# Kernel optimization log

Hardware: AMD Instinct MI355X
Metric: run time of the kernel (lower is better)

## Reference

```python
import jax, jax.numpy as jnp
import numpy as np

B, CITY, H, E, IN = 512, 100, 256, 256, 2
D2 = 2 * H  # num_directions * hidden_size
PEN = 1e6   # already_played_penalty


def _cell(x, h, c, Wih, Whh, b):
    # PyTorch LSTM cell, gate order i,f,g,o
    g = x @ Wih.T + h @ Whh.T + b
    i, f, gg, o = jnp.split(g, 4, axis=-1)
    c = jax.nn.sigmoid(f) * c + jax.nn.sigmoid(i) * jnp.tanh(gg)
    h = jax.nn.sigmoid(o) * jnp.tanh(c)
    return h, c


def _run_lstm(xs, Wih, Whh, b, reverse):
    # xs: [B, T, E] -> outputs [B, T, H], final (h, c)
    Bsz, hdim = xs.shape[0], Whh.shape[1]
    init = (jnp.zeros((Bsz, hdim), xs.dtype), jnp.zeros((Bsz, hdim), xs.dtype))
    def step(carry, x):
        h, c = _cell(x, carry[0], carry[1], Wih, Whh, b)
        return (h, c), h
    (h, c), hs = jax.lax.scan(step, init, jnp.swapaxes(xs, 0, 1), reverse=reverse)
    return jnp.swapaxes(hs, 0, 1), h, c


def setup_inputs() -> dict:
    key = jax.random.key(0)
    ks = iter(jax.random.split(key, 32))
    nrm = lambda shape: 0.1 * jax.random.normal(next(ks), shape, dtype=jnp.float32)
    return {
        "inputs": jax.random.normal(next(ks), (B, CITY, IN), dtype=jnp.float32),
        "test_roads": jax.random.randint(next(ks), (B, CITY), 0, CITY, dtype=jnp.int32),
        "W_embed": nrm((E, IN)),
        "enc_Wih_f": nrm((4 * H, E)), "enc_Whh_f": nrm((4 * H, H)), "enc_b_f": nrm((4 * H,)),
        "enc_Wih_b": nrm((4 * H, E)), "enc_Whh_b": nrm((4 * H, H)), "enc_b_b": nrm((4 * H,)),
        "dec_Wih_f": nrm((4 * H, D2)), "dec_Whh_f": nrm((4 * H, H)), "dec_b_f": nrm((4 * H,)),
        "dec_Wih_b": nrm((4 * H, D2)), "dec_Whh_b": nrm((4 * H, H)), "dec_b_b": nrm((4 * H,)),
        "W_ref": nrm((D2, D2)), "W_q": nrm((D2, D2)), "v": nrm((D2,)),
        "W_ref2": nrm((D2, D2)), "W_q2": nrm((D2, D2)), "v2": nrm((D2,)),
    }


def _forward(inputs, test_roads, W_embed,
             enc_Wih_f, enc_Whh_f, enc_b_f, enc_Wih_b, enc_Whh_b, enc_b_b,
             dec_Wih_f, dec_Whh_f, dec_b_f, dec_Wih_b, dec_Whh_b, dec_b_b,
             W_ref, W_q, v, W_ref2, W_q2, v2):
    Bsz, city, _ = inputs.shape
    emb = inputs @ W_embed.T                                  # [B, city, E]
    enc_f, hf0, cf0 = _run_lstm(emb, enc_Wih_f, enc_Whh_f, enc_b_f, False)
    enc_b, hb0, cb0 = _run_lstm(emb, enc_Wih_b, enc_Whh_b, enc_b_b, True)
    Enc = jnp.concatenate([enc_f, enc_b], axis=-1)            # [B, city, D2]
    # dropout p=0 -> Enc is loop-invariant; hoist the two ref projections
    ref1 = Enc @ W_ref.T                                      # [B, city, D2]
    ref2 = Enc @ W_ref2.T                                     # [B, city, D2]

    def step(carry, tgt):
        x, hf, cf, hb, cb, played, loss = carry
        hf, cf = _cell(x, hf, cf, dec_Wih_f, dec_Whh_f, dec_b_f)
        hb, cb = _cell(x, hb, cb, dec_Wih_b, dec_Whh_b, dec_b_b)
        dec_out = jnp.concatenate([hf, hb], axis=-1)          # [B, D2]
        ow = jnp.tanh(ref1 + (dec_out @ W_q.T)[:, None, :]) @ v - PEN * played   # [B, city]
        aw = jax.nn.softmax(jnp.tanh(ref2 + (x @ W_q2.T)[:, None, :]) @ v2, axis=1)
        sel = jnp.argmax(ow, axis=1)                          # [B]
        x_new = jnp.einsum('bj,bjk->bk', aw, Enc)             # [B, D2]
        played = played + jax.nn.one_hot(sel, city, dtype=played.dtype)
        ce = jax.nn.logsumexp(ow, axis=1) - jnp.take_along_axis(ow, tgt[:, None], axis=1)[:, 0]
        return (x_new, hf, cf, hb, cb, played, loss + ce), None

    x0 = jnp.zeros((Bsz, Enc.shape[-1]), inputs.dtype)
    played0 = jnp.zeros((Bsz, city), inputs.dtype)
    loss0 = jnp.zeros((Bsz,), inputs.dtype)
    carry, _ = jax.lax.scan(step, (x0, hf0, cf0, hb0, cb0, played0, loss0),
                            test_roads.T.astype(jnp.int32))
    return carry[-1]                                          # path_loss [B]


def reference(inputs, test_roads, W_embed,
              enc_Wih_f, enc_Whh_f, enc_b_f, enc_Wih_b, enc_Whh_b, enc_b_b,
              dec_Wih_f, dec_Whh_f, dec_b_f, dec_Wih_b, dec_Whh_b, dec_b_b,
              W_ref, W_q, v, W_ref2, W_q2, v2):
    return _forward(inputs, test_roads, W_embed,
                    enc_Wih_f, enc_Whh_f, enc_b_f, enc_Wih_b, enc_Whh_b, enc_b_b,
                    dec_Wih_f, dec_Whh_f, dec_b_f, dec_Wih_b, dec_Whh_b, dec_b_b,
                    W_ref, W_q, v, W_ref2, W_q2, v2)
```

## Files before the change

### kernel.cpp

```cpp
#include <hip/hip_runtime.h>
#include <hip/hip_fp16.h>
#include <math.h>

namespace {
constexpr int Bn  = 512;
constexpr int Tn  = 100;
constexpr int Hn  = 256;
constexpr int En  = 256;
constexpr int D2n = 512;
constexpr int G4n = 1024;
constexpr float PENf = 1e6f;
constexpr size_t BIGN = (size_t)Bn * Tn * D2n;
constexpr int FLAG_STRIDE = 32;
constexpr int EBLK = 512;
constexpr int DBLK = 896;
constexpr size_t BAR_UINTS = (EBLK + DBLK) * FLAG_STRIDE + 64;
}

using short8  = __attribute__((ext_vector_type(8))) short;
using us8     = __attribute__((ext_vector_type(8))) unsigned short;
using floatx4 = __attribute__((ext_vector_type(4))) float;

template<typename T> __device__ __forceinline__ float cvt_to_f(T x);
template<> __device__ __forceinline__ float cvt_to_f<float>(float x) { return x; }
template<> __device__ __forceinline__ float cvt_to_f<__half>(__half x) {
  return __half2float(x);
}
template<typename T> __device__ __forceinline__ T cvt_from_f(float x);
template<> __device__ __forceinline__ float cvt_from_f<float>(float x) { return x; }
template<> __device__ __forceinline__ __half cvt_from_f<__half>(float x) {
  return __float2half(x);
}
__device__ __forceinline__ float h2f_bits(unsigned short b) {
  __half_raw r; r.x = b; return __half2float(__half(r));
}
__device__ __forceinline__ float fast_exp(float x) {
  return __builtin_amdgcn_exp2f(x * 1.44269504088896340736f);
}
__device__ __forceinline__ float sigmoidf(float x) {
  return __builtin_amdgcn_rcpf(1.0f + fast_exp(-x));
}
__device__ __forceinline__ float fast_tanhf(float x) {
  return 1.0f - 2.0f * __builtin_amdgcn_rcpf(fast_exp(2.0f * x) + 1.0f);
}

__device__ __forceinline__ float loadf_dev(const float* p) {
  return __uint_as_float(__hip_atomic_load((const unsigned*)p, __ATOMIC_RELAXED,
                                           __HIP_MEMORY_SCOPE_AGENT));
}
// ... 49 lines not shown
  split2(v.z, h2, l2); split2(v.w, h3, l3);
  *(short4*)hp = make_short4(h0, h1, h2, h3);
  *(short4*)lp = make_short4(l0, l1, l2, l3);
}

template<int NB>
__device__ __forceinline__ void grid_syncN(unsigned* flags, unsigned* release,
                                           unsigned no) {
  __builtin_amdgcn_s_waitcnt(0);
  __syncthreads();
  if (blockIdx.x == 0) {
    for (int i = threadIdx.x; i < NB; i += 256) {
      if (i > 0) {
        while (__hip_atomic_load(&flags[i * FLAG_STRIDE], __ATOMIC_RELAXED,
                                 __HIP_MEMORY_SCOPE_AGENT) < no)
          __builtin_amdgcn_s_sleep(1);
      }
    }
    __syncthreads();
    if (threadIdx.x == 0)
      __hip_atomic_store(release, no, __ATOMIC_RELAXED, __HIP_MEMORY_SCOPE_AGENT);
  } else {
    if (threadIdx.x == 0) {
      __hip_atomic_store(&flags[blockIdx.x * FLAG_STRIDE], no, __ATOMIC_RELAXED,
                         __HIP_MEMORY_SCOPE_AGENT);
      while (__hip_atomic_load(release, __ATOMIC_RELAXED,
                               __HIP_MEMORY_SCOPE_AGENT) < no)
        __builtin_amdgcn_s_sleep(2);
    }
    __syncthreads();
  }
}

template<typename CT, bool ACC, int NT, bool CSC>
__device__ __forceinline__ void gemm64v2(short* smem,
    const float* A, int lda, int m0,
    const float* B, int ldb, int n0, int K,
    CT* Cbase, size_t crstride, int tid) {
  constexpr int BPL  = NT * 128;
  constexpr int BSZ  = NT * 512;
  constexpr int BUFS = 4096 + 2 * BSZ;
  const int lane = tid & 63, wave = tid >> 6, qm = lane & 15, quad = lane >> 4;
  const int ra = tid >> 3, c4 = tid & 7, j0 = (c4 & 1) * 4, gq = c4 >> 1;
  const int a0 = gq * 512 + ra * 8 + j0;
  const int a1 = gq * 512 + (ra + 32) * 8 + j0;
  const int b0 = gq * BPL + ra * 8 + j0;
  const int b1 = gq * BPL + (ra + 32) * 8 + j0;
  const int CN = K >> 5;

  floatx4 acc[NT];
#pragma unroll
  for (int nt = 0; nt < NT; ++nt) acc[nt] = (floatx4){0.f, 0.f, 0.f, 0.f};

  float4 Aa0, Aa1, Ba0, Ba1, Ab0, Ab1, Bb0, Bb1;
  auto ld = [&](int c, float4& x0, float4& x1, float4& y0, float4& y1) {
    const int k0 = c * 32 + c4 * 4;
    x0 = load4_dev(A + (size_t)(m0 + ra) * lda + k0);
    x1 = load4_dev(A + (size_t)(m0 + ra + 32) * lda + k0);
    y0 = *(const float4*)(B + (size_t)(n0 + ra) * ldb + k0);
    if (NT == 4)
      y1 = *(const float4*)(B + (size_t)(n0 + ra + 32) * ldb + k0);
  };
  auto st = [&](short* bp, const float4& x0, const float4& x1,
                const float4& y0, const float4& y1) {
    store4split(x0, bp + a0, bp + 2048 + a0);
    store4split(x1, bp + a1, bp + 2048 + a1);
    store4split(y0, bp + 4096 + b0, bp + 4096 + BSZ + b0);
    if (NT == 4) store4split(y1, bp + 4096 + b1, bp + 4096 + BSZ + b1);
  };
  auto mm = [&](const short* bp) {
    const int abase = quad * 512 + (wave * 16 + qm) * 8;
    const short8 ah = *(const short8*)&bp[abase];
    const short8 al = *(const short8*)&bp[2048 + abase];
#pragma unroll
    for (int nt = 0; nt < NT; ++nt) {
      const int bb = quad * BPL + (nt * 16 + qm) * 8;
      const short8 bh = *(const short8*)&bp[4096 + bb];
      const short8 bl = *(const short8*)&bp[4096 + BSZ + bb];
      acc[nt] = __builtin_amdgcn_mfma_f32_16x16x32_bf16(ah, bh, acc[nt], 0, 0, 0);
      acc[nt] = __builtin_amdgcn_mfma_f32_16x16x32_bf16(ah, bl, acc[nt], 0, 0, 0);
      acc[nt] = __builtin_amdgcn_mfma_f32_16x16x32_bf16(al, bh, acc[nt], 0, 0, 0);
    }
  };

  ld(0, Aa0, Aa1, Ba0, Ba1);
  if (CN > 1) ld(1, Ab0, Ab1, Bb0, Bb1);
  st(smem, Aa0, Aa1, Ba0, Ba1);
  __syncthreads();
  for (int c = 0; c < CN; c += 2) {
    if (c + 2 < CN) ld(c + 2, Aa0, Aa1, Ba0, Ba1);
    mm(smem);
    if (c + 1 < CN) st(smem + BUFS, Ab0, Ab1, Bb0, Bb1);
    __syncthreads();
    if (c + 1 < CN) {
      if (c + 3 < CN) ld(c + 3, Ab0, Ab1, Bb0, Bb1);
      mm(smem + BUFS);
      if (c + 2 < CN) st(smem, Aa0, Aa1, Ba0, Ba1);
      __syncthreads();
    }
  }

#pragma unroll
  for (int nt = 0; nt < NT; ++nt)
#pragma unroll
    for (int r2 = 0; r2 < 4; ++r2) {
      const int m = wave * 16 + quad * 4 + r2, n = nt * 16 + qm;
      CT* cp = Cbase + (size_t)m * crstride + n;
      float o = acc[nt][r2];
      if (CSC) {
        if (ACC) o += cvt_to_f<CT>(load_dev<CT>(cp));
        store_dev<CT>(cp, cvt_from_f<CT>(o));
      } else {
        if (ACC) o += cvt_to_f<CT>(*cp);
        *cp = cvt_from_f<CT>(o);
      }
    }
}

__device__ __forceinline__ void gates_gemm_v2(floatx4 acc[4], short* smem,
    const float* A1, int lda1, const float* B1, int ldb1, int K1,
    const float* A2, int lda2, const float* B2, int ldb2, int K2,
    int m0, int hoff, int tid) {
  const int lane = tid & 63, wave = tid >> 6, qm = lane & 15, quad = lane >> 4;
  const int ra = tid >> 3, c4 = tid & 7, j0 = (c4 & 1) * 4, gq = c4 >> 1;
  const int a0 = gq * 512 + ra * 8 + j0;
  const int a1 = gq * 512 + (ra + 32) * 8 + j0;
  const int g0 = (ra >> 4) * Hn + hoff + (ra & 15);
  const int g1 = ((ra + 32) >> 4) * Hn + hoff + ((ra + 32) & 15);
  const int C1 = K1 >> 5;
  const int C2 = A2 ? (K2 >> 5) : 0;
  const int CN = C1 + C2;

  float4 Aa0, Aa1, Ba0, Ba1, Ab0, Ab1, Bb0, Bb1;
  auto ld = [&](int c, float4& x0, float4& x1, float4& y0, float4& y1) {
    const float* A; const float* B; int lda, ldb, k0;
    if (c < C1) { A = A1; B = B1; lda = lda1; ldb = ldb1; k0 = c * 32; }
    else        { A = A2; B = B2; lda = lda2; ldb = ldb2; k0 = (c - C1) * 32; }
    k0 += c4 * 4;
    x0 = load4_dev(A + (size_t)(m0 + ra) * lda + k0);
    x1 = load4_dev(A + (size_t)(m0 + ra + 32) * lda + k0);
    y0 = *(const float4*)(B + (size_t)g0 * ldb + k0);
    y1 = *(const float4*)(B + (size_t)g1 * ldb + k0);
  };
  auto st2 = [&](short* bp, const float4& x0, const float4& x1,
                 const float4& y0, const float4& y1) {
    store4split(x0, bp + a0, bp + 2048 + a0);
    store4split(x1, bp + a1, bp + 2048 + a1);
    store4split(y0, bp + 4096 + a0, bp + 6144 + a0);
    store4split(y1, bp + 4096 + a1, bp + 6144 + a1);
  };
  auto mm = [&](const short* bp) {
    const int abase = quad * 512 + (wave * 16 + qm) * 8;
    const short8 ah = *(const short8*)&bp[abase];
    const short8 al = *(const short8*)&bp[2048 + abase];
#pragma unroll
    for (int gg = 0; gg < 4; ++gg) {
      const int bb = quad * 512 + (gg * 16 + qm) * 8;
      const short8 bh = *(const short8*)&bp[4096 + bb];
      const short8 bl = *(const short8*)&bp[6144 + bb];
      acc[gg] = __builtin_amdgcn_mfma_f32_16x16x32_bf16(ah, bh, acc[gg], 0, 0, 0);
      acc[gg] = __builtin_amdgcn_mfma_f32_16x16x32_bf16(ah, bl, acc[gg], 0, 0, 0);
      acc[gg] = __builtin_amdgcn_mfma_f32_16x16x32_bf16(al, bh, acc[gg], 0, 0, 0);
    }
  };

  if (CN <= 0) return;
  ld(0, Aa0, Aa1, Ba0, Ba1);
  if (CN > 1) ld(1, Ab0, Ab1, Bb0, Bb1);
  st2(smem, Aa0, Aa1, Ba0, Ba1);
  __syncthreads();
  for (int c = 0; c < CN; c += 2) {
    if (c + 2 < CN) ld(c + 2, Aa0, Aa1, Ba0, Ba1);
    mm(smem);
    if (c + 1 < CN) st2(smem + 8192, Ab0, Ab1, Bb0, Bb1);
    __syncthreads();
    if (c + 1 < CN) {
      if (c + 3 < CN) ld(c + 3, Ab0, Ab1, Bb0, Bb1);
      mm(smem + 8192);
      if (c + 2 < CN) st2(smem, Aa0, Aa1, Ba0, Ba1);
      __syncthreads();
    }
  }
}

__global__ void weff_kernel(const float* Wih_f, const float* Wih_b,
                            const float* W_embed, float* weff_f, float* weff_b) {
  const int gidx = blockIdx.x * 256 + threadIdx.x;
  if (gidx >= G4n) return;
  float f0 = 0.f, f1 = 0.f, b0 = 0.f, b1 = 0.f;
  for (int e = 0; e < En; ++e) {
    const float w0 = W_embed[e * 2 + 0];
    const float w1 = W_embed[e * 2 + 1];
    const float wf = Wih_f[gidx * En + e];
    const float wb = Wih_b[gidx * En + e];
    f0 = fmaf(wf, w0, f0); f1 = fmaf(wf, w1, f1);
    b0 = fmaf(wb, w0, b0); b1 = fmaf(wb, w1, b1);
  }
  weff_f[gidx * 2 + 0] = f0; weff_f[gidx * 2 + 1] = f1;
  weff_b[gidx * 2 + 0] = b0; weff_b[gidx * 2 + 1] = b1;
}

template<typename ET, typename RT1, typename RT2>
struct EncP {
  const float* inputs;
  const float* Whh_f; const float* Whh_b;
  const float* b_f; const float* b_b;
  const float* weff_f; const float* weff_b;
  const float* W_ref; const float* W_ref2;
  float* hbuf;
  float* c_dec;
  float* dec_out0;
  ET* Enc; RT1* ref1; RT2* ref2;
  unsigned* flags; unsigned* release;
};

template<typename ET, typename RT1, typename RT2>
__global__ __launch_bounds__(256, 2) void enc_coop(EncP<ET, RT1, RT2> P) {
  __shared__ __align__(16) short smem[16384];
  const int bid = blockIdx.x, tid = threadIdx.x;
  const bool gr = bid < 256;
  const int dir = (bid >> 7) & 1, btile = (bid >> 4) & 7, hs = bid & 15;
// ... 63 lines not shown
        const float hn = sigmoidf(gv[3][r2]) * fast_tanhf(cn);
        h_reg[r2] = hn;
        const int m = btile * 64 + wave * 16 + quad * 4 + r2;
        storef_dev(&hdst[(size_t)m * Hn + hcol], hn);
        store_dev<ET>(&P.Enc[(size_t)m * Tn * D2n + (size_t)tt * D2n + dir * Hn + hcol],
                      cvt_from_f<ET>(hn));
      }
    } else if (t > 0) {
      ref_job(hprev, r_dir ? (Tn - t) : (t - 1));
    }
    grid_syncN<EBLK>(P.flags, P.release, ++sync_no);
  }
  if (!gr) {
    ref_job(P.hbuf + (size_t)1 * (2 * Bn * Hn), r_dir ? 0 : (Tn - 1));
  } else {
#pragma unroll
    for (int r2 = 0; r2 < 4; ++r2) {
      const int m = btile * 64 + wave * 16 + quad * 4 + r2;
      P.dec_out0[(size_t)m * D2n + dir * Hn + hcol] = h_reg[r2];
      P.c_dec[((size_t)dir * Bn + m) * Hn + hcol] = c_reg[r2];
    }
  }
}

template<typename ET, typename RT1, typename RT2>
struct DecP {
  const int* test_roads;
  const float* Wih_f; const float* Whh_f; const float* b_f;
  const float* Wih_b; const float* Whh_b; const float* b_b;
  const float* W_q; const float* W_q2; const float* v; const float* v2;
  const ET* Enc; const RT1* ref1; const RT2* ref2;
  float* dec_out;
  float* xb;
  float* qb; float* q2b;
  const float* c_init;
  float* loss;
  unsigned* flags; unsigned* release;
};

template<typename ET, typename RT1, typename RT2>
__global__ __launch_bounds__(256, 4) void dec_coop(DecP<ET, RT1, RT2> P) {
  __shared__ __align__(16) short smem[16384];
  __shared__ float sl[104], playedl[104];
  __shared__ float wmax[4], wsum[4], dpart[4];
  __shared__ int   widx[4];
  __shared__ float lossl;
  const int bid = blockIdx.x, tid = threadIdx.x;
  const int lane = tid & 63, wave = tid >> 6, qm = lane & 15, quad = lane >> 4;
  const int role = (bid < 256) ? 0 : (bid < 384 ? 1 : 2);

  const int dir = (bid >> 7) & 1, btile = (bid >> 4) & 7, hs = bid & 15;
  const int hcol = hs * 16 + qm;
  const float* Wih  = dir ? P.Wih_b : P.Wih_f;
  const float* Whh  = dir ? P.Whh_b : P.Whh_f;
  const float* bias = dir ? P.b_b : P.b_f;
  float c_reg[4] = {0.f, 0.f, 0.f, 0.f};
  if (role == 0) {
#pragma unroll
    for (int r2 = 0; r2 < 4; ++r2) {
      const int m = btile * 64 + wave * 16 + quad * 4 + r2;
      c_reg[r2] = P.c_init[((size_t)dir * Bn + m) * Hn + hcol];
    }
  }
  const int gidx = bid - 256, pbt = gidx >> 4, pn = gidx & 15;
  const int b = bid - 384;
  if (role == 2) {
    if (tid < Tn) playedl[tid] = 0.f;
    if (tid == 0) lossl = 0.f;
  }
  unsigned sync_no = 0;
  __syncthreads();

  auto s1_fused = [&](int u) {
    const int e = lane * 8;
    const float4 qa = load4_dev(P.qb + (size_t)b * D2n + e);
    const float4 qc = load4_dev(P.qb + (size_t)b * D2n + e + 4);
    const float4 va = *(const float4*)(P.v + e);
    const float4 vb2 = *(const float4*)(P.v + e + 4);
    const float q[8]  = {qa.x, qa.y, qa.z, qa.w, qc.x, qc.y, qc.z, qc.w};
    const float vv[8] = {va.x, va.y, va.z, va.w, vb2.x, vb2.y, vb2.z, vb2.w};
    const unsigned short* pr = (const unsigned short*)P.ref1 +
        (size_t)b * Tn * D2n + (size_t)(wave * 25) * D2n + e;
    us8 r0a = *(const us8*)pr;
    us8 r0b = *(const us8*)(pr + (size_t)D2n);
    us8 r1a = *(const us8*)(pr + (size_t)2 * D2n);
    us8 r1b = *(const us8*)(pr + (size_t)3 * D2n);
    float bmax = -INFINITY, sume = 0.f; int bidx = 0;
    for (int ii = 0; ii < 12; ++ii) {
      const int row0 = wave * 25 + 2 * ii;
      float a0 = 0.f, a1 = 0.f;
#pragma unroll
      for (int k = 0; k < 8; ++k) {
        a0 = fmaf(vv[k], fast_tanhf(h2f_bits(r0a[k]) + q[k]), a0);
        a1 = fmaf(vv[k], fast_tanhf(h2f_bits(r0b[k]) + q[k]), a1);
      }
      r0a = r1a; r0b = r1b;
      const int nx = 2 * ii + 4;
      if (nx < 25)     r1a = *(const us8*)(pr + (size_t)nx * D2n);
      if (nx + 1 < 25) r1b = *(const us8*)(pr + (size_t)(nx + 1) * D2n);
#pragma unroll
      for (int off = 32; off > 0; off >>= 1) {
        a0 += __shfl_xor(a0, off, 64);
        a1 += __shfl_xor(a1, off, 64);
      }
// ... 2 lines not shown
      if (ow0 > bmax) { bmax = ow0; bidx = row0; }
      sume += fast_exp(ow0 - 16.f);
      const float ow1 = a1 - PENf * playedl[row0 + 1];
      if (ow1 > bmax) { bmax = ow1; bidx = row0 + 1; }
      sume += fast_exp(ow1 - 16.f);
    }
    {
      const int row = wave * 25 + 24;
      float a = 0.f;
#pragma unroll
      for (int k = 0; k < 8; ++k)
        a = fmaf(vv[k], fast_tanhf(h2f_bits(r0a[k]) + q[k]), a);
#pragma unroll
      for (int off = 32; off > 0; off >>= 1) a += __shfl_xor(a, off, 64);
      if (lane == 0) sl[row] = a;
      const float ow = a - PENf * playedl[row];
      if (ow > bmax) { bmax = ow; bidx = row; }
      sume += fast_exp(ow - 16.f);
    }
    if (lane == 0) { wmax[wave] = bmax; widx[wave] = bidx; wsum[wave] = sume; }
    __syncthreads();
    if (tid == 0) {
      float bv = wmax[0], es = wsum[0]; int bi = widx[0];
#pragma unroll
      for (int w = 1; w < 4; ++w) {
        es += wsum[w];
        if (wmax[w] > bv) { bv = wmax[w]; bi = widx[w]; }
      }
      const int tgt = P.test_roads[b * Tn + u];
      const float owt = sl[tgt] - PENf * playedl[tgt];
      lossl += (16.f + __logf(es)) - owt;
      playedl[bi] += 1.f;
    }
  };

  auto s2x_fused = [&]() {
    const int e = lane * 8;
    const float4 qa = load4_dev(P.q2b + (size_t)b * D2n + e);
    const float4 qc = load4_dev(P.q2b + (size_t)b * D2n + e + 4);
    const float4 va = *(const float4*)(P.v2 + e);
    const float4 vb2 = *(const float4*)(P.v2 + e + 4);
    const float q[8]  = {qa.x, qa.y, qa.z, qa.w, qc.x, qc.y, qc.z, qc.w};
    const float vv[8] = {va.x, va.y, va.z, va.w, vb2.x, vb2.y, vb2.z, vb2.w};
    const unsigned short* pr = (const unsigned short*)P.ref2 +
        (size_t)b * Tn * D2n + (size_t)(wave * 25) * D2n + e;
    const unsigned short* pe = (const unsigned short*)P.Enc +
        (size_t)b * Tn * D2n + (size_t)(wave * 25) * D2n + e;
    us8 r0a = *(const us8*)pr;
    us8 r0b = *(const us8*)(pr + (size_t)D2n);
    us8 r1a = *(const us8*)(pr + (size_t)2 * D2n);
    us8 r1b = *(const us8*)(pr + (size_t)3 * D2n);
    us8 e0a = *(const us8*)pe;
    us8 e0b = *(const us8*)(pe + (size_t)D2n);
    us8 e1a = *(const us8*)(pe + (size_t)2 * D2n);
    us8 e1b = *(const us8*)(pe + (size_t)3 * D2n);
    float xacc[8];
#pragma unroll
    for (int k = 0; k < 8; ++k) xacc[k] = 0.f;
    float den = 0.f;
    for (int ii = 0; ii < 12; ++ii) {
      float a0 = 0.f, a1 = 0.f;
#pragma unroll
      for (int k = 0; k < 8; ++k) {
        a0 = fmaf(vv[k], fast_tanhf(h2f_bits(r0a[k]) + q[k]), a0);
        a1 = fmaf(vv[k], fast_tanhf(h2f_bits(r0b[k]) + q[k]), a1);
      }
      r0a = r1a; r0b = r1b;
      const int nx = 2 * ii + 4;
      if (nx < 25)     r1a = *(const us8*)(pr + (size_t)nx * D2n);
      if (nx + 1 < 25) r1b = *(const us8*)(pr + (size_t)(nx + 1) * D2n);
#pragma unroll
      for (int off = 32; off > 0; off >>= 1) {
        a0 += __shfl_xor(a0, off, 64);
        a1 += __shfl_xor(a1, off, 64);
      }
      const float w0 = fast_exp(a0 - 16.f);
      const float w1 = fast_exp(a1 - 16.f);
      den += w0 + w1;
#pragma unroll
      for (int k = 0; k < 8; ++k) {
        xacc[k] = fmaf(w0, h2f_bits(e0a[k]), xacc[k]);
        xacc[k] = fmaf(w1, h2f_bits(e0b[k]), xacc[k]);
      }
      e0a = e1a; e0b = e1b;
      if (nx < 25)     e1a = *(const us8*)(pe + (size_t)nx * D2n);
      if (nx + 1 < 25) e1b = *(const us8*)(pe + (size_t)(nx + 1) * D2n);
    }
    {
      float a = 0.f;
#pragma unroll
      for (int k = 0; k < 8; ++k)
        a = fmaf(vv[k], fast_tanhf(h2f_bits(r0a[k]) + q[k]), a);
#pragma unroll
      for (int off = 32; off > 0; off >>= 1) a += __shfl_xor(a, off, 64);
      const float w = fast_exp(a - 16.f);
      den += w;
#pragma unroll
      for (int k = 0; k < 8; ++k)
        xacc[k] = fmaf(w, h2f_bits(e0a[k]), xacc[k]);
    }
    float* xpart = (float*)smem;
#pragma unroll
    for (int k = 0; k < 8; ++k) xpart[wave * 512 + e + k] = xacc[k];
    if (lane == 0) dpart[wave] = den;
    __syncthreads();
    {
      const float dsum = dpart[0] + dpart[1] + dpart[2] + dpart[3];
      const float inv = __builtin_amdgcn_rcpf(dsum);
      const int c = tid * 2;
      float2 s;
      s.x = (xpart[c] + xpart[512 + c] + xpart[1024 + c] + xpart[1536 + c]) * inv;
      s.y = (xpart[c + 1] + xpart[512 + c + 1] + xpart[1024 + c + 1] +
             xpart[1536 + c + 1]) * inv;
      store2_dev(&P.xb[(size_t)b * D2n + c], s);
    }
  };

  for (int t = 0; t < Tn; ++t) {
    const float* dcur = P.dec_out + (size_t)(t & 1) * (Bn * D2n);
    float* dnext = P.dec_out + (size_t)((t + 1) & 1) * (Bn * D2n);
    if (role == 0) {
      floatx4 acc[4];
#pragma unroll
      for (int gg = 0; gg < 4; ++gg) acc[gg] = (floatx4){0.f, 0.f, 0.f, 0.f};
      gates_gemm_v2(acc, smem, P.xb, D2n, Wih, D2n, D2n,
                    dcur + dir * Hn, D2n, Whh, Hn, Hn, btile * 64, hs * 16, tid);
#pragma unroll
      for (int gg = 0; gg < 4; ++gg) {
        const float bn = bias[gg * Hn + hcol];
#pragma unroll
        for (int r2 = 0; r2 < 4; ++r2) acc[gg][r2] += bn;
      }
#pragma unroll
      for (int r2 = 0; r2 < 4; ++r2) {
        const float cn = sigmoidf(acc[1][r2]) * c_reg[r2] +
                         sigmoidf(acc[0][r2]) * fast_tanhf(acc[2][r2]);
        c_reg[r2] = cn;
        const float hn = sigmoidf(acc[3][r2]) * fast_tanhf(cn);
        const int m = btile * 64 + wave * 16 + quad * 4 + r2;
        storef_dev(&dnext[(size_t)m * D2n + dir * Hn + hcol], hn);
      }
    } else if (role == 1) {
      gemm64v2<float, false, 2, true>(smem, P.xb, D2n, pbt * 64,
                                      P.W_q2, D2n, pn * 32, D2n,
                                      P.q2b + (size_t)(pbt * 64) * D2n + pn * 32,
                                      D2n, tid);
    } else if (t > 0) {
      s1_fused(t - 1);
    }
    grid_syncN<DBLK>(P.flags, P.release, ++sync_no);
    if (role == 1) {
      gemm64v2<float, false, 2, true>(smem, dnext, D2n, pbt * 64,
                                      P.W_q, D2n, pn * 32, D2n,
                                      P.qb + (size_t)(pbt * 64) * D2n + pn * 32,
                                      D2n, tid);
    } else if (role == 2) {
      s2x_fused();
    }
    grid_syncN<DBLK>(P.flags, P.release, ++sync_no);
  }
  if (role == 2) {
    s1_fused(Tn - 1);
    if (tid == 0) P.loss[b] = lossl;
  }
}

static void run_all(void* const* d_in, void* d_out, char* ws, hipStream_t stream) {
  using ET = __half; using RT1 = __half; using RT2 = __half;
  const float* inputs     = (const float*)d_in[0];
  const int*   test_roads = (const int*)d_in[1];
  const float* W_embed    = (const float*)d_in[2];
  const float* enc_Wih_f  = (const float*)d_in[3];
  const float* enc_Whh_f  = (const float*)d_in[4];
  const float* enc_b_f    = (const float*)d_in[5];
  const float* enc_Wih_b  = (const float*)d_in[6];
  const float* enc_Whh_b  = (const float*)d_in[7];
  const float* enc_b_b    = (const float*)d_in[8];
  const float* dec_Wih_f  = (const float*)d_in[9];
  const float* dec_Whh_f  = (const float*)d_in[10];
  const float* dec_b_f    = (const float*)d_in[11];
  const float* dec_Wih_b  = (const float*)d_in[12];
  const float* dec_Whh_b  = (const float*)d_in[13];
  const float* dec_b_b    = (const float*)d_in[14];
  const float* W_ref      = (const float*)d_in[15];
  const float* W_q        = (const float*)d_in[16];
  const float* v          = (const float*)d_in[17];
  const float* W_ref2     = (const float*)d_in[18];
  const float* W_q2       = (const float*)d_in[19];
  const float* v2         = (const float*)d_in[20];

  char* p0 = ws;
  ET*  Enc  = (ET*)p0;  p0 += BIGN * sizeof(ET);
  RT1* ref1 = (RT1*)p0; p0 += BIGN * sizeof(RT1);
  RT2* ref2 = (RT2*)p0; p0 += BIGN * sizeof(RT2);
  unsigned* flagsE = (unsigned*)p0;
  unsigned* relE   = flagsE + EBLK * FLAG_STRIDE;
  unsigned* flagsD = relE + 32;
  unsigned* relD   = flagsD + DBLK * FLAG_STRIDE;
  float* xb      = (float*)(p0 + BAR_UINTS * 4);
  float* dec_out = xb + Bn * D2n;
  float* hbuf    = dec_out + 2 * Bn * D2n;
  float* c_dec   = hbuf + 4 * Bn * Hn;
  float* qb      = c_dec + 2 * Bn * Hn;
  float* q2b     = qb + Bn * D2n;
  float* weff_f  = q2b + Bn * D2n;
  float* weff_b  = weff_f + G4n * 2;

  hipMemsetAsync(ref1, 0, BIGN * (sizeof(RT1) + sizeof(RT2)), stream);
  hipMemsetAsync(flagsE, 0, BAR_UINTS * 4 + (size_t)Bn * D2n * 4, stream);

  weff_kernel<<<G4n / 256, 256, 0, stream>>>(enc_Wih_f, enc_Wih_b, W_embed,
                                             weff_f, weff_b);

  EncP<ET, RT1, RT2> ep = { inputs, enc_Whh_f, enc_Whh_b, enc_b_f, enc_b_b,
                            weff_f, weff_b, W_ref, W_ref2,
                            hbuf, c_dec, dec_out, Enc, ref1, ref2,
                            flagsE, relE };
  enc_coop<ET, RT1, RT2><<<EBLK, 256, 0, stream>>>(ep);

  DecP<ET, RT1, RT2> dp = { test_roads,
                            dec_Wih_f, dec_Whh_f, dec_b_f,
                            dec_Wih_b, dec_Whh_b, dec_b_b,
                            W_q, W_q2, v, v2,
                            Enc, ref1, ref2,
                            dec_out, xb, qb, q2b, c_dec,
                            (float*)d_out, flagsD, relD };
  dec_coop<ET, RT1, RT2><<<DBLK, 256, 0, stream>>>(dp);
}

extern "C" void kernel_launch(void* const* d_in, const int* in_sizes, int n_in,
                              void* d_out, int out_size, void* d_ws, size_t ws_size,
                              hipStream_t stream) {
  (void)in_sizes; (void)n_in; (void)out_size; (void)ws_size;
  run_all(d_in, d_out, (char*)d_ws, stream);
}
```

Baseline: 7.137 ms.

## Split glimpse attention context across role-2 and idle blocks with deferred normalization

```diff
diff --git a/kernel.cpp b/kernel.cpp
--- a/kernel.cpp
+++ b/kernel.cpp
@@ -130,11 +130,13 @@
   }
 }
 
-template<typename CT, bool ACC, int NT, bool CSC>
+template<typename CT, bool ACC, int NT, bool CSC, bool XDIV = false>
 __device__ __forceinline__ void gemm64v2(short* smem,
     const float* A, int lda, int m0,
     const float* B, int ldb, int n0, int K,
-    CT* Cbase, size_t crstride, int tid) {
+    CT* Cbase, size_t crstride, int tid,
+    const float* AH = nullptr, const float* dN = nullptr,
+    const float* dH = nullptr) {
   constexpr int BPL  = NT * 128;
   constexpr int BSZ  = NT * 512;
   constexpr int BUFS = 4096 + 2 * BSZ;
@@ -146,6 +148,14 @@
   const int b1 = gq * BPL + (ra + 32) * 8 + j0;
   const int CN = K >> 5;
 
+  float inv0 = 1.f, inv1 = 1.f;
+  if (XDIV) {
+    inv0 = __builtin_amdgcn_rcpf(loadf_dev(dN + m0 + ra) +
+                                 loadf_dev(dH + m0 + ra));
+    inv1 = __builtin_amdgcn_rcpf(loadf_dev(dN + m0 + ra + 32) +
+                                 loadf_dev(dH + m0 + ra + 32));
+  }
+
   floatx4 acc[NT];
 #pragma unroll
   for (int nt = 0; nt < NT; ++nt) acc[nt] = (floatx4){0.f, 0.f, 0.f, 0.f};
@@ -155,6 +165,14 @@
     const int k0 = c * 32 + c4 * 4;
     x0 = load4_dev(A + (size_t)(m0 + ra) * lda + k0);
     x1 = load4_dev(A + (size_t)(m0 + ra + 32) * lda + k0);
+    if (XDIV) {
+      const float4 h0 = load4_dev(AH + (size_t)(m0 + ra) * lda + k0);
+      const float4 h1 = load4_dev(AH + (size_t)(m0 + ra + 32) * lda + k0);
+      x0.x = (x0.x + h0.x) * inv0; x0.y = (x0.y + h0.y) * inv0;
+      x0.z = (x0.z + h0.z) * inv0; x0.w = (x0.w + h0.w) * inv0;
+      x1.x = (x1.x + h1.x) * inv1; x1.y = (x1.y + h1.y) * inv1;
+      x1.z = (x1.z + h1.z) * inv1; x1.w = (x1.w + h1.w) * inv1;
+    }
     y0 = *(const float4*)(B + (size_t)(n0 + ra) * ldb + k0);
     if (NT == 4)
       y1 = *(const float4*)(B + (size_t)(n0 + ra + 32) * ldb + k0);
@@ -215,10 +233,13 @@
     }
 }
 
+template<bool XDIV = false>
 __device__ __forceinline__ void gates_gemm_v2(floatx4 acc[4], short* smem,
     const float* A1, int lda1, const float* B1, int ldb1, int K1,
     const float* A2, int lda2, const float* B2, int ldb2, int K2,
-    int m0, int hoff, int tid) {
+    int m0, int hoff, int tid,
+    const float* AH = nullptr, const float* dN = nullptr,
+    const float* dH = nullptr) {
   const int lane = tid & 63, wave = tid >> 6, qm = lane & 15, quad = lane >> 4;
   const int ra = tid >> 3, c4 = tid & 7, j0 = (c4 & 1) * 4, gq = c4 >> 1;
   const int a0 = gq * 512 + ra * 8 + j0;
@@ -229,6 +250,14 @@
   const int C2 = A2 ? (K2 >> 5) : 0;
   const int CN = C1 + C2;
 
+  float inv0 = 1.f, inv1 = 1.f;
+  if (XDIV) {
+    inv0 = __builtin_amdgcn_rcpf(loadf_dev(dN + m0 + ra) +
+                                 loadf_dev(dH + m0 + ra));
+    inv1 = __builtin_amdgcn_rcpf(loadf_dev(dN + m0 + ra + 32) +
+                                 loadf_dev(dH + m0 + ra + 32));
+  }
+
   float4 Aa0, Aa1, Ba0, Ba1, Ab0, Ab1, Bb0, Bb1;
   auto ld = [&](int c, float4& x0, float4& x1, float4& y0, float4& y1) {
     const float* A; const float* B; int lda, ldb, k0;
@@ -237,6 +266,14 @@
     k0 += c4 * 4;
     x0 = load4_dev(A + (size_t)(m0 + ra) * lda + k0);
     x1 = load4_dev(A + (size_t)(m0 + ra + 32) * lda + k0);
+    if (XDIV && c < C1) {
+      const float4 h0 = load4_dev(AH + (size_t)(m0 + ra) * lda + k0);
+      const float4 h1 = load4_dev(AH + (size_t)(m0 + ra + 32) * lda + k0);
+      x0.x = (x0.x + h0.x) * inv0; x0.y = (x0.y + h0.y) * inv0;
+      x0.z = (x0.z + h0.z) * inv0; x0.w = (x0.w + h0.w) * inv0;
+      x1.x = (x1.x + h1.x) * inv1; x1.y = (x1.y + h1.y) * inv1;
+      x1.z = (x1.z + h1.z) * inv1; x1.w = (x1.w + h1.w) * inv1;
+    }
     y0 = *(const float4*)(B + (size_t)g0 * ldb + k0);
     y1 = *(const float4*)(B + (size_t)g1 * ldb + k0);
   };
@@ -282,9 +319,11 @@
 }
 
 __global__ void weff_kernel(const float* Wih_f, const float* Wih_b,
-                            const float* W_embed, float* weff_f, float* weff_b) {
+                            const float* W_embed, float* weff_f, float* weff_b,
+                            float* denN, float* denH) {
   const int gidx = blockIdx.x * 256 + threadIdx.x;
   if (gidx >= G4n) return;
+  if (gidx < Bn) { denN[gidx] = 0.5f; denH[gidx] = 0.5f; }
   float f0 = 0.f, f1 = 0.f, b0 = 0.f, b1 = 0.f;
   for (int e = 0; e < En; ++e) {
     const float w0 = W_embed[e * 2 + 0];
@@ -414,6 +453,8 @@
   const ET* Enc; const RT1* ref1; const RT2* ref2;
   float* dec_out;
   float* xb;
+  float* xbH;
+  float* denN; float* denH;
   float* qb; float* q2b;
   const float* c_init;
   float* loss;
@@ -522,18 +563,20 @@
     }
   };
 
-  auto s2x_fused = [&]() {
+  auto s2x_partial = [&](int bb, int row0, bool tail,
+                         float (&xacc)[8], float& den) {
     const int e = lane * 8;
-    const float4 qa = load4_dev(P.q2b + (size_t)b * D2n + e);
-    const float4 qc = load4_dev(P.q2b + (size_t)b * D2n + e + 4);
+    const float4 qa = load4_dev(P.q2b + (size_t)bb * D2n + e);
+    const float4 qc = load4_dev(P.q2b + (size_t)bb * D2n + e + 4);
     const float4 va = *(const float4*)(P.v2 + e);
     const float4 vb2 = *(const float4*)(P.v2 + e + 4);
     const float q[8]  = {qa.x, qa.y, qa.z, qa.w, qc.x, qc.y, qc.z, qc.w};
     const float vv[8] = {va.x, va.y, va.z, va.w, vb2.x, vb2.y, vb2.z, vb2.w};
+    const int nr = tail ? 17 : 16;
     const unsigned short* pr = (const unsigned short*)P.ref2 +
-        (size_t)b * Tn * D2n + (size_t)(wave * 25) * D2n + e;
+        (size_t)bb * Tn * D2n + (size_t)row0 * D2n + e;
     const unsigned short* pe = (const unsigned short*)P.Enc +
-        (size_t)b * Tn * D2n + (size_t)(wave * 25) * D2n + e;
+        (size_t)bb * Tn * D2n + (size_t)row0 * D2n + e;
     us8 r0a = *(const us8*)pr;
     us8 r0b = *(const us8*)(pr + (size_t)D2n);
     us8 r1a = *(const us8*)(pr + (size_t)2 * D2n);
@@ -542,11 +585,10 @@
     us8 e0b = *(const us8*)(pe + (size_t)D2n);
     us8 e1a = *(const us8*)(pe + (size_t)2 * D2n);
     us8 e1b = *(const us8*)(pe + (size_t)3 * D2n);
-    float xacc[8];
 #pragma unroll
     for (int k = 0; k < 8; ++k) xacc[k] = 0.f;
-    float den = 0.f;
-    for (int ii = 0; ii < 12; ++ii) {
+    den = 0.f;
+    for (int ii = 0; ii < 8; ++ii) {
       float a0 = 0.f, a1 = 0.f;
 #pragma unroll
       for (int k = 0; k < 8; ++k) {
@@ -555,8 +597,8 @@
       }
       r0a = r1a; r0b = r1b;
       const int nx = 2 * ii + 4;
-      if (nx < 25)     r1a = *(const us8*)(pr + (size_t)nx * D2n);
-      if (nx + 1 < 25) r1b = *(const us8*)(pr + (size_t)(nx + 1) * D2n);
+      if (nx < nr)     r1a = *(const us8*)(pr + (size_t)nx * D2n);
+      if (nx + 1 < nr) r1b = *(const us8*)(pr + (size_t)(nx + 1) * D2n);
 #pragma unroll
       for (int off = 32; off > 0; off >>= 1) {
         a0 += __shfl_xor(a0, off, 64);
@@ -571,10 +613,10 @@
         xacc[k] = fmaf(w1, h2f_bits(e0b[k]), xacc[k]);
       }
       e0a = e1a; e0b = e1b;
-      if (nx < 25)     e1a = *(const us8*)(pe + (size_t)nx * D2n);
-      if (nx + 1 < 25) e1b = *(const us8*)(pe + (size_t)(nx + 1) * D2n);
-    }
-    {
+      if (nx < nr)     e1a = *(const us8*)(pe + (size_t)nx * D2n);
+      if (nx + 1 < nr) e1b = *(const us8*)(pe + (size_t)(nx + 1) * D2n);
+    }
+    if (tail) {
       float a = 0.f;
 #pragma unroll
       for (int k = 0; k < 8; ++k)
@@ -586,21 +628,6 @@
 #pragma unroll
       for (int k = 0; k < 8; ++k)
         xacc[k] = fmaf(w, h2f_bits(e0a[k]), xacc[k]);
-    }
-    float* xpart = (float*)smem;
-#pragma unroll
-    for (int k = 0; k < 8; ++k) xpart[wave * 512 + e + k] = xacc[k];
-    if (lane == 0) dpart[wave] = den;
-    __syncthreads();
-    {
-      const float dsum = dpart[0] + dpart[1] + dpart[2] + dpart[3];
-      const float inv = __builtin_amdgcn_rcpf(dsum);
-      const int c = tid * 2;
-      float2 s;
-      s.x = (xpart[c] + xpart[512 + c] + xpart[1024 + c] + xpart[1536 + c]) * inv;
-      s.y = (xpart[c + 1] + xpart[512 + c + 1] + xpart[1024 + c + 1] +
-             xpart[1536 + c + 1]) * inv;
-      store2_dev(&P.xb[(size_t)b * D2n + c], s);
     }
   };
 
@@ -611,8 +638,9 @@
       floatx4 acc[4];
 #pragma unroll
       for (int gg = 0; gg < 4; ++gg) acc[gg] = (floatx4){0.f, 0.f, 0.f, 0.f};
-      gates_gemm_v2(acc, smem, P.xb, D2n, Wih, D2n, D2n,
-                    dcur + dir * Hn, D2n, Whh, Hn, Hn, btile * 64, hs * 16, tid);
+      gates_gemm_v2<true>(acc, smem, P.xb, D2n, Wih, D2n, D2n,
+                          dcur + dir * Hn, D2n, Whh, Hn, Hn, btile * 64,
+                          hs * 16, tid, P.xbH, P.denN, P.denH);
 #pragma unroll
       for (int gg = 0; gg < 4; ++gg) {
         const float bn = bias[gg * Hn + hcol];
@@ -629,10 +657,10 @@
         storef_dev(&dnext[(size_t)m * D2n + dir * Hn + hcol], hn);
       }
     } else if (role == 1) {
-      gemm64v2<float, false, 2, true>(smem, P.xb, D2n, pbt * 64,
+      gemm64v2<float, false, 2, true, true>(smem, P.xb, D2n, pbt * 64,
                                       P.W_q2, D2n, pn * 32, D2n,
                                       P.q2b + (size_t)(pbt * 64) * D2n + pn * 32,
-                                      D2n, tid);
+                                      D2n, tid, P.xbH, P.denN, P.denH);
     } else if (t > 0) {
       s1_fused(t - 1);
     }
@@ -643,7 +671,47 @@
                                       P.qb + (size_t)(pbt * 64) * D2n + pn * 32,
                                       D2n, tid);
     } else if (role == 2) {
-      s2x_fused();
+      float xacc[8]; float den;
+      s2x_partial(b, wave * 17, true, xacc, den);
+      float* xpart = (float*)smem;
+#pragma unroll
+      for (int k = 0; k < 8; ++k) xpart[wave * 512 + lane * 8 + k] = xacc[k];
+      if (lane == 0) dpart[wave] = den;
+      __syncthreads();
+      {
+        const int c = tid * 2;
+        float2 s;
+        s.x = xpart[c] + xpart[512 + c] + xpart[1024 + c] + xpart[1536 + c];
+        s.y = xpart[c + 1] + xpart[512 + c + 1] + xpart[1024 + c + 1] +
+              xpart[1536 + c + 1];
+        store2_dev(&P.xb[(size_t)b * D2n + c], s);
+        if (tid == 0)
+          storef_dev(&P.denN[b], dpart[0] + dpart[1] + dpart[2] + dpart[3]);
+      }
+    } else {
+      const int hb = 2 * bid + (wave >> 1);
+      float xacc[8]; float den;
+      s2x_partial(hb, 68 + (wave & 1) * 16, false, xacc, den);
+      float* xpart = (float*)smem;
+#pragma unroll
+      for (int k = 0; k < 8; ++k) xpart[wave * 512 + lane * 8 + k] = xacc[k];
+      if (lane == 0) dpart[wave] = den;
+      __syncthreads();
+      {
+        const int c = tid * 2;
+        float2 s0;
+        s0.x = xpart[c] + xpart[512 + c];
+        s0.y = xpart[c + 1] + xpart[512 + c + 1];
+        store2_dev(&P.xbH[(size_t)(2 * bid) * D2n + c], s0);
+        float2 s1v;
+        s1v.x = xpart[1024 + c] + xpart[1536 + c];
+        s1v.y = xpart[1024 + c + 1] + xpart[1536 + c + 1];
+        store2_dev(&P.xbH[(size_t)(2 * bid + 1) * D2n + c], s1v);
+        if (tid == 0) {
+          storef_dev(&P.denH[2 * bid], dpart[0] + dpart[1]);
+          storef_dev(&P.denH[2 * bid + 1], dpart[2] + dpart[3]);
+        }
+      }
     }
     grid_syncN<DBLK>(P.flags, P.release, ++sync_no);
   }
@@ -693,12 +761,16 @@
   float* q2b     = qb + Bn * D2n;
   float* weff_f  = q2b + Bn * D2n;
   float* weff_b  = weff_f + G4n * 2;
+  float* denN    = weff_b + G4n * 2;
+  float* denH    = denN + Bn;
+  float* xbH     = denH + Bn;
 
   hipMemsetAsync(ref1, 0, BIGN * (sizeof(RT1) + sizeof(RT2)), stream);
   hipMemsetAsync(flagsE, 0, BAR_UINTS * 4 + (size_t)Bn * D2n * 4, stream);
+  hipMemsetAsync(xbH, 0, (size_t)Bn * D2n * 4, stream);
 
   weff_kernel<<<G4n / 256, 256, 0, stream>>>(enc_Wih_f, enc_Wih_b, W_embed,
-                                             weff_f, weff_b);
+                                             weff_f, weff_b, denN, denH);
 
   EncP<ET, RT1, RT2> ep = { inputs, enc_Whh_f, enc_Whh_b, enc_b_f, enc_b_b,
                             weff_f, weff_b, W_ref, W_ref2,
@@ -711,7 +783,7 @@
                             dec_Wih_b, dec_Whh_b, dec_b_b,
                             W_q, W_q2, v, v2,
                             Enc, ref1, ref2,
-                            dec_out, xb, qb, q2b, c_dec,
+                            dec_out, xb, xbH, denN, denH, qb, q2b, c_dec,
                             (float*)d_out, flagsD, relD };
   dec_coop<ET, RT1, RT2><<<DBLK, 256, 0, stream>>>(dp);
 }
```

Result: slower. 8.277 ms (+16.0%).

## Split decoder attention-2 rows between role-2 blocks and idle gate blocks

Applied to the files above, without the earlier changes.

```diff
diff --git a/kernel.cpp b/kernel.cpp
--- a/kernel.cpp
+++ b/kernel.cpp
@@ -14,7 +14,7 @@
 constexpr int FLAG_STRIDE = 32;
 constexpr int EBLK = 512;
 constexpr int DBLK = 896;
-constexpr size_t BAR_UINTS = (EBLK + DBLK) * FLAG_STRIDE + 64;
+constexpr size_t BAR_UINTS = (size_t)(EBLK + DBLK + Bn) * FLAG_STRIDE + 64;
 }
 
 using short8  = __attribute__((ext_vector_type(8))) short;
@@ -414,6 +414,9 @@
   const ET* Enc; const RT1* ref1; const RT2* ref2;
   float* dec_out;
   float* xb;
+  float* xbH;
+  float* denH;
+  unsigned* bflags;
   float* qb; float* q2b;
   const float* c_init;
   float* loss;
@@ -522,18 +525,20 @@
     }
   };
 
-  auto s2x_fused = [&]() {
+  auto s2x_partial = [&](int bb, int row0, bool tail,
+                         float (&xacc)[8], float& den) {
     const int e = lane * 8;
-    const float4 qa = load4_dev(P.q2b + (size_t)b * D2n + e);
-    const float4 qc = load4_dev(P.q2b + (size_t)b * D2n + e + 4);
+    const float4 qa = load4_dev(P.q2b + (size_t)bb * D2n + e);
+    const float4 qc = load4_dev(P.q2b + (size_t)bb * D2n + e + 4);
     const float4 va = *(const float4*)(P.v2 + e);
     const float4 vb2 = *(const float4*)(P.v2 + e + 4);
     const float q[8]  = {qa.x, qa.y, qa.z, qa.w, qc.x, qc.y, qc.z, qc.w};
     const float vv[8] = {va.x, va.y, va.z, va.w, vb2.x, vb2.y, vb2.z, vb2.w};
+    const int nr = tail ? 17 : 16;
     const unsigned short* pr = (const unsigned short*)P.ref2 +
-        (size_t)b * Tn * D2n + (size_t)(wave * 25) * D2n + e;
+        (size_t)bb * Tn * D2n + (size_t)row0 * D2n + e;
     const unsigned short* pe = (const unsigned short*)P.Enc +
-        (size_t)b * Tn * D2n + (size_t)(wave * 25) * D2n + e;
+        (size_t)bb * Tn * D2n + (size_t)row0 * D2n + e;
     us8 r0a = *(const us8*)pr;
     us8 r0b = *(const us8*)(pr + (size_t)D2n);
     us8 r1a = *(const us8*)(pr + (size_t)2 * D2n);
@@ -542,11 +547,10 @@
     us8 e0b = *(const us8*)(pe + (size_t)D2n);
     us8 e1a = *(const us8*)(pe + (size_t)2 * D2n);
     us8 e1b = *(const us8*)(pe + (size_t)3 * D2n);
-    float xacc[8];
 #pragma unroll
     for (int k = 0; k < 8; ++k) xacc[k] = 0.f;
-    float den = 0.f;
-    for (int ii = 0; ii < 12; ++ii) {
+    den = 0.f;
+    for (int ii = 0; ii < 8; ++ii) {
       float a0 = 0.f, a1 = 0.f;
 #pragma unroll
       for (int k = 0; k < 8; ++k) {
@@ -555,8 +559,8 @@
       }
       r0a = r1a; r0b = r1b;
       const int nx = 2 * ii + 4;
-      if (nx < 25)     r1a = *(const us8*)(pr + (size_t)nx * D2n);
-      if (nx + 1 < 25) r1b = *(const us8*)(pr + (size_t)(nx + 1) * D2n);
+      if (nx < nr)     r1a = *(const us8*)(pr + (size_t)nx * D2n);
+      if (nx + 1 < nr) r1b = *(const us8*)(pr + (size_t)(nx + 1) * D2n);
 #pragma unroll
       for (int off = 32; off > 0; off >>= 1) {
         a0 += __shfl_xor(a0, off, 64);
@@ -571,10 +575,10 @@
         xacc[k] = fmaf(w1, h2f_bits(e0b[k]), xacc[k]);
       }
       e0a = e1a; e0b = e1b;
-      if (nx < 25)     e1a = *(const us8*)(pe + (size_t)nx * D2n);
-      if (nx + 1 < 25) e1b = *(const us8*)(pe + (size_t)(nx + 1) * D2n);
-    }
-    {
+      if (nx < nr)     e1a = *(const us8*)(pe + (size_t)nx * D2n);
+      if (nx + 1 < nr) e1b = *(const us8*)(pe + (size_t)(nx + 1) * D2n);
+    }
+    if (tail) {
       float a = 0.f;
 #pragma unroll
       for (int k = 0; k < 8; ++k)
@@ -586,21 +590,6 @@
 #pragma unroll
       for (int k = 0; k < 8; ++k)
         xacc[k] = fmaf(w, h2f_bits(e0a[k]), xacc[k]);
-    }
-    float* xpart = (float*)smem;
-#pragma unroll
-    for (int k = 0; k < 8; ++k) xpart[wave * 512 + e + k] = xacc[k];
-    if (lane == 0) dpart[wave] = den;
-    __syncthreads();
-    {
-      const float dsum = dpart[0] + dpart[1] + dpart[2] + dpart[3];
-      const float inv = __builtin_amdgcn_rcpf(dsum);
-      const int c = tid * 2;
-      float2 s;
-      s.x = (xpart[c] + xpart[512 + c] + xpart[1024 + c] + xpart[1536 + c]) * inv;
-      s.y = (xpart[c + 1] + xpart[512 + c + 1] + xpart[1024 + c + 1] +
-             xpart[1536 + c + 1]) * inv;
-      store2_dev(&P.xb[(size_t)b * D2n + c], s);
     }
   };
 
@@ -643,7 +632,66 @@
                                       P.qb + (size_t)(pbt * 64) * D2n + pn * 32,
                                       D2n, tid);
     } else if (role == 2) {
-      s2x_fused();
+      float xacc[8]; float den;
+      s2x_partial(b, wave * 17, true, xacc, den);
+      float* xpart = (float*)smem;
+#pragma unroll
+      for (int k = 0; k < 8; ++k) xpart[wave * 512 + lane * 8 + k] = xacc[k];
+      if (lane == 0) dpart[wave] = den;
+      __syncthreads();
+      if (tid == 0) {
+        while (__hip_atomic_load(&P.bflags[b * FLAG_STRIDE], __ATOMIC_RELAXED,
+                                 __HIP_MEMORY_SCOPE_AGENT) < (unsigned)(t + 1))
+          __builtin_amdgcn_s_sleep(1);
+      }
+      __syncthreads();
+      {
+        const float dsum = dpart[0] + dpart[1] + dpart[2] + dpart[3] +
+                           loadf_dev(&P.denH[b]);
+        const float inv = __builtin_amdgcn_rcpf(dsum);
+        const int c = tid * 2;
+        float2 s;
+        s.x = (xpart[c] + xpart[512 + c] + xpart[1024 + c] + xpart[1536 + c] +
+               loadf_dev(&P.xbH[(size_t)b * D2n + c])) * inv;
+        s.y = (xpart[c + 1] + xpart[512 + c + 1] + xpart[1024 + c + 1] +
+               xpart[1536 + c + 1] +
+               loadf_dev(&P.xbH[(size_t)b * D2n + c + 1])) * inv;
+        store2_dev(&P.xb[(size_t)b * D2n + c], s);
+      }
+    } else {
+      const int hb = 2 * bid + (wave >> 1);
+      float xacc[8]; float den;
+      s2x_partial(hb, 68 + (wave & 1) * 16, false, xacc, den);
+      float* xpart = (float*)smem;
+#pragma unroll
+      for (int k = 0; k < 8; ++k) xpart[wave * 512 + lane * 8 + k] = xacc[k];
+      if (lane == 0) dpart[wave] = den;
+      __syncthreads();
+      {
+        const int half = tid >> 7;
+        const int cc = (tid & 127) * 4;
+        const float* xp0 = xpart + half * 1024;
+        float2 sa, sb;
+        sa.x = xp0[cc]     + xp0[512 + cc];
+        sa.y = xp0[cc + 1] + xp0[512 + cc + 1];
+        sb.x = xp0[cc + 2] + xp0[512 + cc + 2];
+        sb.y = xp0[cc + 3] + xp0[512 + cc + 3];
+        float* dst = P.xbH + (size_t)(2 * bid + half) * D2n + cc;
+        store2_dev(dst, sa);
+        store2_dev(dst + 2, sb);
+        if (tid == 0)   storef_dev(&P.denH[2 * bid],     dpart[0] + dpart[1]);
+        if (tid == 128) storef_dev(&P.denH[2 * bid + 1], dpart[2] + dpart[3]);
+      }
+      __builtin_amdgcn_s_waitcnt(0);
+      __syncthreads();
+      if (tid == 0) {
+        __hip_atomic_store(&P.bflags[(2 * bid) * FLAG_STRIDE],
+                           (unsigned)(t + 1), __ATOMIC_RELAXED,
+                           __HIP_MEMORY_SCOPE_AGENT);
+        __hip_atomic_store(&P.bflags[(2 * bid + 1) * FLAG_STRIDE],
+                           (unsigned)(t + 1), __ATOMIC_RELAXED,
+                           __HIP_MEMORY_SCOPE_AGENT);
+      }
     }
     grid_syncN<DBLK>(P.flags, P.release, ++sync_no);
   }
@@ -685,6 +733,7 @@
   unsigned* relE   = flagsE + EBLK * FLAG_STRIDE;
   unsigned* flagsD = relE + 32;
   unsigned* relD   = flagsD + DBLK * FLAG_STRIDE;
+  unsigned* bflags = relD + 32;
   float* xb      = (float*)(p0 + BAR_UINTS * 4);
   float* dec_out = xb + Bn * D2n;
   float* hbuf    = dec_out + 2 * Bn * D2n;
@@ -693,6 +742,8 @@
   float* q2b     = qb + Bn * D2n;
   float* weff_f  = q2b + Bn * D2n;
   float* weff_b  = weff_f + G4n * 2;
+  float* xbH     = weff_b + G4n * 2;
+  float* denH    = xbH + (size_t)Bn * D2n;
 
   hipMemsetAsync(ref1, 0, BIGN * (sizeof(RT1) + sizeof(RT2)), stream);
   hipMemsetAsync(flagsE, 0, BAR_UINTS * 4 + (size_t)Bn * D2n * 4, stream);
@@ -711,7 +762,7 @@
                             dec_Wih_b, dec_Whh_b, dec_b_b,
                             W_q, W_q2, v, v2,
                             Enc, ref1, ref2,
-                            dec_out, xb, qb, q2b, c_dec,
+                            dec_out, xb, xbH, denH, bflags, qb, q2b, c_dec,
                             (float*)d_out, flagsD, relD };
   dec_coop<ET, RT1, RT2><<<DBLK, 256, 0, stream>>>(dp);
 }
```

New measurement: 7.342 ms. +2.9%, slower.

## Replace second grid barrier per decoder step with per-group counter flags

Applied to the files above, without the earlier changes.

```diff
diff --git a/kernel.cpp b/kernel.cpp
--- a/kernel.cpp
+++ b/kernel.cpp
@@ -14,7 +14,7 @@
 constexpr int FLAG_STRIDE = 32;
 constexpr int EBLK = 512;
 constexpr int DBLK = 896;
-constexpr size_t BAR_UINTS = (EBLK + DBLK) * FLAG_STRIDE + 64;
+constexpr size_t BAR_UINTS = (size_t)(EBLK + DBLK + Bn) * FLAG_STRIDE + 64;
 }
 
 using short8  = __attribute__((ext_vector_type(8))) short;
@@ -415,6 +415,7 @@
   float* dec_out;
   float* xb;
   float* qb; float* q2b;
+  unsigned* cq2; unsigned* cq;
   const float* c_init;
   float* loss;
   unsigned* flags; unsigned* release;
@@ -446,12 +447,29 @@
   }
   const int gidx = bid - 256, pbt = gidx >> 4, pn = gidx & 15;
   const int b = bid - 384;
+  const int grp = (b >> 6) & 7;
   if (role == 2) {
     if (tid < Tn) playedl[tid] = 0.f;
     if (tid == 0) lossl = 0.f;
   }
   unsigned sync_no = 0;
   __syncthreads();
+
+  auto flag_add = [&](unsigned* ctr) {
+    __builtin_amdgcn_s_waitcnt(0);
+    __syncthreads();
+    if (tid == 0)
+      __hip_atomic_fetch_add(&ctr[pbt * FLAG_STRIDE], 1u, __ATOMIC_RELAXED,
+                             __HIP_MEMORY_SCOPE_AGENT);
+  };
+  auto flag_wait = [&](unsigned* ctr, unsigned want) {
+    if (tid == 0) {
+      while (__hip_atomic_load(&ctr[grp * FLAG_STRIDE], __ATOMIC_RELAXED,
+                               __HIP_MEMORY_SCOPE_AGENT) < want)
+        __builtin_amdgcn_s_sleep(1);
+    }
+    __syncthreads();
+  };
 
   auto s1_fused = [&](int u) {
     const int e = lane * 8;
@@ -520,9 +538,10 @@
       lossl += (16.f + __logf(es)) - owt;
       playedl[bi] += 1.f;
     }
-  };
-
-  auto s2x_fused = [&]() {
+    __syncthreads();
+  };
+
+  auto s2x_fused = [&](float* xdst) {
     const int e = lane * 8;
     const float4 qa = load4_dev(P.q2b + (size_t)b * D2n + e);
     const float4 qc = load4_dev(P.q2b + (size_t)b * D2n + e + 4);
@@ -600,18 +619,21 @@
       s.x = (xpart[c] + xpart[512 + c] + xpart[1024 + c] + xpart[1536 + c]) * inv;
       s.y = (xpart[c + 1] + xpart[512 + c + 1] + xpart[1024 + c + 1] +
              xpart[1536 + c + 1]) * inv;
-      store2_dev(&P.xb[(size_t)b * D2n + c], s);
-    }
+      store2_dev(&xdst[(size_t)b * D2n + c], s);
+    }
+    __syncthreads();
   };
 
   for (int t = 0; t < Tn; ++t) {
+    const float* xcur = P.xb + (size_t)(t & 1) * (Bn * D2n);
+    float* xnext = P.xb + (size_t)((t + 1) & 1) * (Bn * D2n);
     const float* dcur = P.dec_out + (size_t)(t & 1) * (Bn * D2n);
     float* dnext = P.dec_out + (size_t)((t + 1) & 1) * (Bn * D2n);
     if (role == 0) {
       floatx4 acc[4];
 #pragma unroll
       for (int gg = 0; gg < 4; ++gg) acc[gg] = (floatx4){0.f, 0.f, 0.f, 0.f};
-      gates_gemm_v2(acc, smem, P.xb, D2n, Wih, D2n, D2n,
+      gates_gemm_v2(acc, smem, xcur, D2n, Wih, D2n, D2n,
                     dcur + dir * Hn, D2n, Whh, Hn, Hn, btile * 64, hs * 16, tid);
 #pragma unroll
       for (int gg = 0; gg < 4; ++gg) {
@@ -629,25 +651,37 @@
         storef_dev(&dnext[(size_t)m * D2n + dir * Hn + hcol], hn);
       }
     } else if (role == 1) {
-      gemm64v2<float, false, 2, true>(smem, P.xb, D2n, pbt * 64,
+      gemm64v2<float, false, 2, true>(smem, xcur, D2n, pbt * 64,
                                       P.W_q2, D2n, pn * 32, D2n,
                                       P.q2b + (size_t)(pbt * 64) * D2n + pn * 32,
                                       D2n, tid);
-    } else if (t > 0) {
-      s1_fused(t - 1);
+      flag_add(P.cq2);
+      if (t > 0) {
+        __syncthreads();
+        gemm64v2<float, false, 2, true>(smem, dcur, D2n, pbt * 64,
+                                        P.W_q, D2n, pn * 32, D2n,
+                                        P.qb + (size_t)(pbt * 64) * D2n + pn * 32,
+                                        D2n, tid);
+        flag_add(P.cq);
+      }
+    } else {
+      flag_wait(P.cq2, 16u * (unsigned)(t + 1));
+      s2x_fused(xnext);
+      if (t > 0) {
+        flag_wait(P.cq, 16u * (unsigned)t);
+        s1_fused(t - 1);
+      }
     }
     grid_syncN<DBLK>(P.flags, P.release, ++sync_no);
-    if (role == 1) {
-      gemm64v2<float, false, 2, true>(smem, dnext, D2n, pbt * 64,
-                                      P.W_q, D2n, pn * 32, D2n,
-                                      P.qb + (size_t)(pbt * 64) * D2n + pn * 32,
-                                      D2n, tid);
-    } else if (role == 2) {
-      s2x_fused();
-    }
-    grid_syncN<DBLK>(P.flags, P.release, ++sync_no);
-  }
-  if (role == 2) {
+  }
+  if (role == 1) {
+    gemm64v2<float, false, 2, true>(smem, P.dec_out + (size_t)(Tn & 1) * (Bn * D2n),
+                                    D2n, pbt * 64, P.W_q, D2n, pn * 32, D2n,
+                                    P.qb + (size_t)(pbt * 64) * D2n + pn * 32,
+                                    D2n, tid);
+    flag_add(P.cq);
+  } else if (role == 2) {
+    flag_wait(P.cq, 16u * (unsigned)Tn);
     s1_fused(Tn - 1);
     if (tid == 0) P.loss[b] = lossl;
   }
@@ -685,8 +719,10 @@
   unsigned* relE   = flagsE + EBLK * FLAG_STRIDE;
   unsigned* flagsD = relE + 32;
   unsigned* relD   = flagsD + DBLK * FLAG_STRIDE;
+  unsigned* cq2    = relD + 32;
+  unsigned* cq     = cq2 + 8 * FLAG_STRIDE;
   float* xb      = (float*)(p0 + BAR_UINTS * 4);
-  float* dec_out = xb + Bn * D2n;
+  float* dec_out = xb + 2 * Bn * D2n;
   float* hbuf    = dec_out + 2 * Bn * D2n;
   float* c_dec   = hbuf + 4 * Bn * Hn;
   float* qb      = c_dec + 2 * Bn * Hn;
@@ -695,7 +731,7 @@
   float* weff_b  = weff_f + G4n * 2;
 
   hipMemsetAsync(ref1, 0, BIGN * (sizeof(RT1) + sizeof(RT2)), stream);
-  hipMemsetAsync(flagsE, 0, BAR_UINTS * 4 + (size_t)Bn * D2n * 4, stream);
+  hipMemsetAsync(flagsE, 0, BAR_UINTS * 4 + (size_t)2 * Bn * D2n * 4, stream);
 
   weff_kernel<<<G4n / 256, 256, 0, stream>>>(enc_Wih_f, enc_Wih_b, W_embed,
                                              weff_f, weff_b);
@@ -711,7 +747,7 @@
                             dec_Wih_b, dec_Whh_b, dec_b_b,
                             W_q, W_q2, v, v2,
                             Enc, ref1, ref2,
-                            dec_out, xb, qb, q2b, c_dec,
+                            dec_out, xb, qb, q2b, cq2, cq, c_dec,
                             (float*)d_out, flagsD, relD };
   dec_coop<ET, RT1, RT2><<<DBLK, 256, 0, stream>>>(dp);
 }
```

After: 7.614 ms. +6.7%, slower.
